# Performance work log

Measured on AMD Instinct MI355X. Metric: run time of the kernel, lower is better.

Reference implementation:

```python
import jax, jax.numpy as jnp
import numpy as np

DECAY = 0.99
EPS = 1e-05
TEMP = 1.0


def setup_inputs() -> dict:
    key = jax.random.key(0)
    k1, k2, k3 = jax.random.split(key, 3)
    B, T, D, C = 64, 512, 256, 1024
    x = jax.random.normal(k1, (B, T, D), dtype=jnp.float32)
    embed = jax.random.normal(k2, (1, C, D), dtype=jnp.float32)
    embed_avg = jax.random.normal(k3, (1, C, D), dtype=jnp.float32)
    cluster_size = jnp.ones((1, C), dtype=jnp.float32)
    return {"x": x, "embed": embed, "embed_avg": embed_avg, "cluster_size": cluster_size}


def reference(x, embed, embed_avg, cluster_size):
    B, T, D = x.shape
    H, C, _ = embed.shape  # H = num_codebooks = 1
    flatten = x.reshape(H, B * T, D)  # pack_one 'h * d'
    e = jax.lax.stop_gradient(embed)  # learnable_codebook = False

    dist = (2.0 * jnp.einsum('hnd,hcd->hnc', flatten, e)
            - jnp.sum(flatten * flatten, axis=-1, keepdims=True)
            - jnp.sum(e * e, axis=-1)[:, None, :])  # [h, N, C]

    # gumbel_sample: deterministic argmax + straight-through one-hot
    embed_ind = jnp.argmax(dist, axis=-1)  # [h, N]
    probs = jax.nn.softmax(dist / TEMP, axis=-1)
    hard = jax.nn.one_hot(embed_ind, C, dtype=dist.dtype)
    embed_onehot = probs + jax.lax.stop_gradient(hard - probs)  # [h, N, C]

    # quantize via onehot matmul (training path)
    quantize = jnp.einsum('hnc,hcd->hnd', embed_onehot, e).reshape(B, T, D)

    # EMA codebook update
    cs_new = DECAY * cluster_size + (1.0 - DECAY) * embed_onehot.sum(axis=1)  # [h, C]
    embed_sum = jnp.einsum('hnd,hnc->hcd', flatten, embed_onehot)  # [h, C, D]
    ea_new = DECAY * embed_avg + (1.0 - DECAY) * embed_sum
    n = jnp.sum(cs_new, axis=-1, keepdims=True)
    cs_smoothed = (cs_new + EPS) / (n + C * EPS) * n  # laplace smoothing * n
    embed_norm = ea_new / cs_smoothed[..., None]  # new codebook [h, C, D]

    return (quantize, embed_ind.reshape(B, T), embed_norm, cs_new)
```

## Files before the change

### kernel.cpp

```cpp
#include <hip/hip_runtime.h>
#include <cstdint>

#define DECAY 0.99f
#define OMD   0.01f
#define EPSV  1e-5f

constexpr int N_PTS   = 32768;
constexpr int D_DIM   = 256;
constexpr int C_CODES = 1024;
constexpr int NKT     = 12;
constexpr int AP      = 512;
constexpr int BP      = 512;

constexpr int PG = 8;
constexpr int PK = 8;
constexpr int LCAP = 4096;

typedef _Float16 half8  __attribute__((ext_vector_type(8)));
typedef _Float16 half4v __attribute__((ext_vector_type(4)));
typedef float    floatx4 __attribute__((ext_vector_type(4)));

constexpr size_t WS_ENORM = 0;
constexpr size_t WS_FCNT  = 1024;
constexpr size_t WS_XNORM = 2048;
constexpr size_t WS_PCNT  = 34816;
constexpr size_t WS_CAND4 = 43008;
constexpr size_t WS_FLAGR = WS_CAND4 + 1048576;
constexpr size_t WS_CAND2 = WS_FLAGR + 32768;
constexpr size_t WS_A16   = WS_CAND2 + 1048576;
constexpr size_t WS_B16   = WS_A16 + 8388608;
constexpr size_t WS_TOTAL_FLOATS = WS_B16 + 262144;

__device__ __forceinline__ void async_copy16(const void* g, void* s) {
    __builtin_amdgcn_global_load_lds(
        (const __attribute__((address_space(1))) unsigned int*)(uintptr_t)g,
        (__attribute__((address_space(3))) unsigned int*)(uintptr_t)s, 16, 0, 0);
}

__device__ __forceinline__ unsigned ord_u32(float v) {
    unsigned s = __float_as_uint(v);
    unsigned m = (unsigned)((int)s >> 31);
    return s ^ (m | 0x80000000u);
}
__device__ __forceinline__ float ord_dec(unsigned t) {
    unsigned s = (t & 0x80000000u) ? (t ^ 0x80000000u) : ~t;
    return __uint_as_float(s);
}

__global__ __launch_bounds__(256) void vq_prep(const float* __restrict__ X,
                                               const float* __restrict__ E,
                                               _Float16* __restrict__ A,
                                               _Float16* __restrict__ B,
                                               float* __restrict__ enorm,
                                               float* __restrict__ xnorm,
                                               int* __restrict__ fcnt) {
    if (blockIdx.x < 8192) {
        int i = blockIdx.x * 256 + threadIdx.x;
        int n = i >> 6, kq = (i & 63) * 4;
        float4 v = reinterpret_cast<const float4*>(X)[i];
        _Float16 h0 = (_Float16)v.x, h1 = (_Float16)v.y, h2 = (_Float16)v.z, h3 = (_Float16)v.w;
        _Float16 l0 = (_Float16)(v.x - (float)h0), l1 = (_Float16)(v.y - (float)h1);
        _Float16 l2 = (_Float16)(v.z - (float)h2), l3 = (_Float16)(v.w - (float)h3);
        half4v hi = {h0, h1, h2, h3};
        half4v lo = {l0, l1, l2, l3};
        _Float16* row = A + (size_t)n * AP;
        *reinterpret_cast<half4v*>(row + kq)       = hi;
        *reinterpret_cast<half4v*>(row + 256 + kq) = lo;
        float s = v.x * v.x + v.y * v.y + v.z * v.z + v.w * v.w;
        int lane = threadIdx.x & 63;
#pragma unroll
        for (int off = 32; off > 0; off >>= 1) s += __shfl_down(s, off, 64);
        if (lane == 0) xnorm[n] = s;
    } else {
        if (blockIdx.x == 8192 && threadIdx.x == 0) *fcnt = 0;
        int i = (blockIdx.x - 8192) * 256 + threadIdx.x;
        int c = i >> 6, kq = (i & 63) * 4;
        float4 v = reinterpret_cast<const float4*>(E)[i];
        _Float16 h0 = (_Float16)v.x, h1 = (_Float16)v.y, h2 = (_Float16)v.z, h3 = (_Float16)v.w;
        _Float16 l0 = (_Float16)(v.x - (float)h0), l1 = (_Float16)(v.y - (float)h1);
        _Float16 l2 = (_Float16)(v.z - (float)h2), l3 = (_Float16)(v.w - (float)h3);
        half4v hi = {h0, h1, h2, h3};
        half4v lo = {l0, l1, l2, l3};
        _Float16* row = B + (size_t)c * BP;
        *reinterpret_cast<half4v*>(row + kq)       = hi;
        *reinterpret_cast<half4v*>(row + 256 + kq) = lo;
        float s = v.x * v.x + v.y * v.y + v.z * v.z + v.w * v.w;
        int lane = threadIdx.x & 63;
#pragma unroll
        for (int off = 32; off > 0; off >>= 1) s += __shfl_down(s, off, 64);
        if (lane == 0) enorm[c] = s;
    }
}

__global__ __launch_bounds__(256) void vq_enorm(const float* __restrict__ E,
                                                float* __restrict__ enorm) {
    int c    = blockIdx.x * 4 + (threadIdx.x >> 6);
    int lane = threadIdx.x & 63;
    float4 v = reinterpret_cast<const float4*>(E)[c * 64 + lane];
    float s  = v.x * v.x + v.y * v.y + v.z * v.z + v.w * v.w;
#pragma unroll
    for (int off = 32; off > 0; off >>= 1) s += __shfl_down(s, off, 64);
    if (lane == 0) enorm[c] = s;
}

#define TOP2_DPP(CTRL)                                                          \
    {                                                                           \
        unsigned o1 = (unsigned)__builtin_amdgcn_update_dpp((int)k1, (int)k1,   \
                                                            CTRL, 0xF, 0xF, false); \
        unsigned o2 = (unsigned)__builtin_amdgcn_update_dpp((int)k2, (int)k2,   \
                                                            CTRL, 0xF, 0xF, false); \
        unsigned tmn = o1 < k1 ? o1 : k1;                                       \
        k1 = o1 > k1 ? o1 : k1;                                                 \
        k2 = o2 > k2 ? o2 : k2;                                                 \
        k2 = tmn > k2 ? tmn : k2;                                               \
    }

__global__ __launch_bounds__(256, 2) void vq_gemm1(
    const _Float16* __restrict__ A, const _Float16* __restrict__ B,
    const float* __restrict__ enorm, float4* __restrict__ cand4) {
    __shared__ _Float16 As[128 * 64];
    __shared__ _Float16 Bs[256 * 64];

    const int L  = blockIdx.x;
    const int ct = (L >> 3) & 3;
    const int rt = (L & 7) | ((L >> 5) << 3);
    const int n0  = rt * 128;
    const int cb0 = ct * 256;

    const int tid = threadIdx.x;
    const int w   = tid >> 6;
    const int l   = tid & 63;

    const int srow = l >> 3;
    const int sq   = (l & 7) ^ srow;

    floatx4 acc[4][8] = {};

    for (int kt = 0; kt < 4; ++kt) {
        const int k0 = kt * 64;
        __syncthreads();
#pragma unroll
        for (int t = 0; t < 4; ++t) {
            int rr = w * 32 + t * 8;
            const _Float16* ga = A + (size_t)(n0 + rr + srow) * AP + k0 + sq * 8;
            async_copy16(ga, &As[rr * 64]);
        }
#pragma unroll
        for (int t = 0; t < 8; ++t) {
            int rr = w * 64 + t * 8;
            const _Float16* gb = B + (size_t)(cb0 + rr + srow) * BP + k0 + sq * 8;
            async_copy16(gb, &Bs[rr * 64]);
        }
        __syncthreads();
#pragma unroll
        for (int kk = 0; kk < 2; ++kk) {
            half8 af[4], bf[8];
            int qa = kk * 4 + (l >> 4);
#pragma unroll
            for (int i = 0; i < 4; ++i) {
                int row = (w & 1) * 64 + 16 * i + (l & 15);
                af[i] = *reinterpret_cast<const half8*>(&As[row * 64 + (qa ^ (row & 7)) * 8]);
            }
#pragma unroll
            for (int j = 0; j < 8; ++j) {
                int crow = (w >> 1) * 128 + 16 * j + (l & 15);
                bf[j] = *reinterpret_cast<const half8*>(&Bs[crow * 64 + (qa ^ (crow & 7)) * 8]);
            }
#pragma unroll
            for (int i = 0; i < 4; ++i)
#pragma unroll
                for (int j = 0; j < 8; ++j)
                    acc[i][j] = __builtin_amdgcn_mfma_f32_16x16x32_f16(af[i], bf[j], acc[i][j], 0, 0, 0);
        }
    }

    const int colbase = cb0 + (w >> 1) * 128 + (l & 15);
    float    en[8];
    unsigned idxenc[8];
#pragma unroll
    for (int j = 0; j < 8; ++j) {
        en[j]     = enorm[colbase + 16 * j];
        idxenc[j] = 1023u - (unsigned)(colbase + 16 * j);
    }

#pragma unroll
    for (int i = 0; i < 4; ++i) {
#pragma unroll
        for (int reg = 0; reg < 4; ++reg) {
            unsigned k1 = 0u, k2 = 0u;
#pragma unroll
            for (int j = 0; j < 8; ++j) {
                float v = 2.0f * acc[i][j][reg] - en[j];
                unsigned key = (ord_u32(v) & 0xFFFFFC00u) | idxenc[j];
                unsigned tmn = key < k1 ? key : k1;
                k1 = key > k1 ? key : k1;
                k2 = tmn > k2 ? tmn : k2;
            }
            TOP2_DPP(0xB1)
            TOP2_DPP(0x4E)
            TOP2_DPP(0x141)
            TOP2_DPP(0x140)
            if ((l & 15) == 0) {
                unsigned c1 = 1023u - (k1 & 1023u);
                float v1 = ord_dec(k1 & 0xFFFFFC00u);
                float v2 = ord_dec(k2 & 0xFFFFFC00u);
                int row = n0 + (w & 1) * 64 + 16 * i + (l >> 4) * 4 + reg;
                cand4[(size_t)row * 8 + ct * 2 + (w >> 1)] =
                    make_float4(v1, (float)c1, v2, 0.0f);
            }
        }
    }
}

__global__ __launch_bounds__(256) void vq_merge3f(
    const float4* __restrict__ cand4, const float* __restrict__ E,
    const float* __restrict__ enorm, const float* __restrict__ xnorm,
    float* __restrict__ quant, float* __restrict__ indout,
    int* __restrict__ flagrows, int* __restrict__ fcnt) {
    __shared__ int   rowsel[64];
    __shared__ float emred[256];
    const int tid = threadIdx.x;
    const int n0  = blockIdx.x * 64;

    float em = fmaxf(fmaxf(enorm[tid], enorm[tid + 256]),
                     fmaxf(enorm[tid + 512], enorm[tid + 768]));
    emred[tid] = em;
    __syncthreads();
    for (int st = 128; st > 0; st >>= 1) {
        if (tid < st) emred[tid] = fmaxf(emred[tid], emred[tid + st]);
        __syncthreads();
    }
    const float emax = emred[0];

    if (tid < 64) {
        int r = n0 + tid;
        float b1 = -3.4e38f, b2 = -3.4e38f;
        int   i1 = 0x7fffffff;
#pragma unroll
        for (int t = 0; t < 8; ++t) {
            float4 cv = cand4[(size_t)r * 8 + t];
            int ci = (int)cv.y;
            if (cv.x > b1 || (cv.x == b1 && ci < i1)) { b2 = fmaxf(b1, cv.z); b1 = cv.x; i1 = ci; }
            else b2 = fmaxf(b2, cv.x);
        }
        i1 &= (C_CODES - 1);
        rowsel[tid] = i1;
        indout[r]   = (float)i1;
        float T = 0.004150390625f * sqrtf(xnorm[r] * emax)
                + 0.0001220703125f * emax + 0.5f;
        if (b1 - b2 <= T) { int p = atomicAdd(fcnt, 1); flagrows[p] = r; }
    }
    __syncthreads();

    const float4* E4 = reinterpret_cast<const float4*>(E);
    float4*       Q4 = reinterpret_cast<float4*>(quant);
    const int lane = tid & 63;
#pragma unroll
    for (int it = 0; it < 16; ++it) {
        int r   = (tid >> 6) + 4 * it;
        int idx = rowsel[r];
        Q4[(n0 + r) * 64 + lane] = E4[idx * 64 + lane];
    }
}

__global__ __launch_bounds__(256, 2) void vq_gemm2(
    const _Float16* __restrict__ A, const _Float16* __restrict__ B,
    const float* __restrict__ enorm, const int* __restrict__ flagrows,
    const int* __restrict__ fcnt, float2* __restrict__ cand2) {
    const int fc = *fcnt;

    const int L      = blockIdx.x;
    const int within = L >> 3;
    const int ct     = within & 7;
    const int rt     = (L & 7) | ((within >> 3) << 3);
    const int n0     = rt * 128;
    if (n0 >= fc) return;
    const int cb0    = ct * 128;

    __shared__ _Float16 As[128 * 64];
    __shared__ _Float16 Bs[128 * 64];

    const int tid = threadIdx.x;
    const int w   = tid >> 6;
    const int l   = tid & 63;
    const int srow = l >> 3;
    const int sq   = (l & 7) ^ srow;

    int grow[4];
#pragma unroll
    for (int t = 0; t < 4; ++t) {
        int slot = n0 + w * 32 + t * 8 + srow;
        int r    = (slot < fc) ? flagrows[slot] : 0;
        grow[t]  = r & (N_PTS - 1);
    }

    floatx4 acc[4][4] = {};

    for (int kt = 0; kt < NKT; ++kt) {
        const int ka = ((kt < 8) ? (kt & 3) : (kt - 4)) * 64;
        const int kb = (kt < 4) ? kt * 64 : (kt < 8 ? 256 + (kt - 4) * 64 : (kt - 8) * 64);
        __syncthreads();
#pragma unroll
        for (int t = 0; t < 4; ++t) {
            int rr = w * 32 + t * 8;
            const _Float16* ga = A + (size_t)grow[t] * AP + ka + sq * 8;
            async_copy16(ga, &As[rr * 64]);
            const _Float16* gb = B + (size_t)(cb0 + rr + srow) * BP + kb + sq * 8;
            async_copy16(gb, &Bs[rr * 64]);
        }
        __syncthreads();
#pragma unroll
        for (int kk = 0; kk < 2; ++kk) {
            half8 af[4], bf[4];
            int qa = kk * 4 + (l >> 4);
#pragma unroll
            for (int i = 0; i < 4; ++i) {
                int row  = (w & 1) * 64 + 16 * i + (l & 15);
                af[i] = *reinterpret_cast<const half8*>(&As[row * 64 + (qa ^ (row & 7)) * 8]);
                int crow = (w >> 1) * 64 + 16 * i + (l & 15);
                bf[i] = *reinterpret_cast<const half8*>(&Bs[crow * 64 + (qa ^ (crow & 7)) * 8]);
            }
#pragma unroll
            for (int i = 0; i < 4; ++i)
#pragma unroll
                for (int j = 0; j < 4; ++j)
                    acc[i][j] = __builtin_amdgcn_mfma_f32_16x16x32_f16(af[i], bf[j], acc[i][j], 0, 0, 0);
        }
    }

    const int colbase = cb0 + (w >> 1) * 64 + (l & 15);
    float en[4];
#pragma unroll
    for (int j = 0; j < 4; ++j) en[j] = enorm[colbase + 16 * j];

#pragma unroll
    for (int i = 0; i < 4; ++i) {
#pragma unroll
        for (int reg = 0; reg < 4; ++reg) {
            float bv = -3.4e38f;
            int   bi = 0x7fffffff;
#pragma unroll
            for (int j = 0; j < 4; ++j) {
                float v = 2.0f * acc[i][j][reg] - en[j];
                int   c = colbase + 16 * j;
                if (v > bv || (v == bv && c < bi)) { bv = v; bi = c; }
            }
#pragma unroll
            for (int s = 1; s < 16; s <<= 1) {
                float ov = __shfl_xor(bv, s, 64);
                int   oi = __shfl_xor(bi, s, 64);
                if (ov > bv || (ov == bv && oi < bi)) { bv = ov; bi = oi; }
            }
            if ((l & 15) == 0) {
                int slot = n0 + (w & 1) * 64 + 16 * i + (l >> 4) * 4 + reg;
                cand2[(size_t)slot * 16 + ct * 2 + (w >> 1)] = make_float2(bv, (float)bi);
            }
        }
    }
}

__global__ __launch_bounds__(256) void vq_patch(
    const float2* __restrict__ cand2, const int* __restrict__ flagrows,
    const int* __restrict__ fcnt, const float* __restrict__ E,
    float* __restrict__ quant, float* __restrict__ indout) {
    int fc = *fcnt;
    if (fc > N_PTS) fc = N_PTS;
    const int s0 = blockIdx.x * 64;
    if (s0 >= fc) return;

    __shared__ int rowsel[64];
    __shared__ int rowid[64];
    const int tid = threadIdx.x;
    if (tid < 64) {
        int s = s0 + tid;
        if (s < fc) {
            int r = flagrows[s] & (N_PTS - 1);
            float bv = -3.4e38f;
            int   bi = 0x7fffffff;
#pragma unroll
            for (int t = 0; t < 16; ++t) {
                float2 cv = cand2[(size_t)s * 16 + t];
                int ci = (int)cv.y;
                if (cv.x > bv || (cv.x == bv && ci < bi)) { bv = cv.x; bi = ci; }
            }
            bi &= (C_CODES - 1);
            rowsel[tid] = bi;
            rowid[tid]  = r;
            indout[r]   = (float)bi;
        } else {
            rowsel[tid] = -1;
            rowid[tid]  = 0;
        }
    }
    __syncthreads();

    const float4* E4 = reinterpret_cast<const float4*>(E);
    float4*       Q4 = reinterpret_cast<float4*>(quant);
    const int lane = tid & 63;
#pragma unroll
    for (int it = 0; it < 16; ++it) {
        int rs  = (tid >> 6) + 4 * it;
        int idx = rowsel[rs];
        if (idx >= 0) Q4[(size_t)rowid[rs] * 64 + lane] = E4[idx * 64 + lane];
    }
}

__global__ __launch_bounds__(256) void vq_part(
    const float* __restrict__ X, const float* __restrict__ indf,
    float* __restrict__ P, int* __restrict__ pcnt) {
    __shared__ int list[LCAP];
    __shared__ int cnt[PK];
    __shared__ int lcnt;
    const int cg = blockIdx.x;
    const int g  = blockIdx.y;
    const int t  = threadIdx.x;
    if (t == 0) lcnt = 0;
    if (t < PK) cnt[t] = 0;
    __syncthreads();

    const float4* I4 = reinterpret_cast<const float4*>(indf);
    float4 v[4];
#pragma unroll
    for (int j = 0; j < 4; ++j)
        v[j] = I4[g * 1024 + j * 256 + t];

#pragma unroll
    for (int j = 0; j < 4; ++j) {
        int base = (g * 1024 + j * 256 + t) * 4;
        int k0 = (int)v[j].x, k1 = (int)v[j].y, k2 = (int)v[j].z, k3 = (int)v[j].w;
        if ((k0 >> 3) == cg) { int p = atomicAdd(&lcnt, 1); atomicAdd(&cnt[k0 & 7], 1); if (p < LCAP) list[p] = ((base + 0) << 3) | (k0 & 7); }
        if ((k1 >> 3) == cg) { int p = atomicAdd(&lcnt, 1); atomicAdd(&cnt[k1 & 7], 1); if (p < LCAP) list[p] = ((base + 1) << 3) | (k1 & 7); }
        if ((k2 >> 3) == cg) { int p = atomicAdd(&lcnt, 1); atomicAdd(&cnt[k2 & 7], 1); if (p < LCAP) list[p] = ((base + 2) << 3) | (k2 & 7); }
        if ((k3 >> 3) == cg) { int p = atomicAdd(&lcnt, 1); atomicAdd(&cnt[k3 & 7], 1); if (p < LCAP) list[p] = ((base + 3) << 3) | (k3 & 7); }
    }
    __syncthreads();

    int m = lcnt; if (m > LCAP) m = LCAP;
    float acc[PK] = {0, 0, 0, 0, 0, 0, 0, 0};
    int r = 0;
    for (; r + 8 <= m; r += 8) {
        int e[8];
        float val[8];
#pragma unroll
        for (int q = 0; q < 8; ++q) e[q] = list[r + q];
#pragma unroll
        for (int q = 0; q < 8; ++q) val[q] = X[(size_t)(e[q] >> 3) * D_DIM + t];
#pragma unroll
        for (int q = 0; q < 8; ++q) {
            int k = e[q] & 7;
#pragma unroll
            for (int kk = 0; kk < PK; ++kk) acc[kk] += (k == kk) ? val[q] : 0.0f;
        }
    }
    for (; r < m; ++r) {
        int e = list[r];
        float val = X[(size_t)(e >> 3) * D_DIM + t];
        int k = e & 7;
#pragma unroll
        for (int kk = 0; kk < PK; ++kk) acc[kk] += (k == kk) ? val : 0.0f;
    }

#pragma unroll
    for (int kk = 0; kk < PK; ++kk)
        P[((size_t)g * C_CODES + cg * PK + kk) * D_DIM + t] = acc[kk];
    if (t < PK) pcnt[g * C_CODES + cg * PK + t] = cnt[t];
}

__global__ __launch_bounds__(256) void vq_comb(
    const float* __restrict__ P, const int* __restrict__ pcnt,
    const float* __restrict__ ea, const float* __restrict__ cs_in,
    float* __restrict__ emb_norm, float* __restrict__ cs_out) {
    __shared__ float red[256];
    const int c = blockIdx.x;
    const int t = threadIdx.x;
    red[t] = cs_in[t] + cs_in[t + 256] + cs_in[t + 512] + cs_in[t + 768];
    __syncthreads();
    for (int st = 128; st > 0; st >>= 1) {
        if (t < st) red[t] += red[t + st];
        __syncthreads();
    }
    const float cssum = red[0];

    float s = 0.0f;
#pragma unroll
    for (int g = 0; g < PG; ++g)
        s += P[((size_t)g * C_CODES + c) * D_DIM + t];
    int total = 0;
#pragma unroll
    for (int g = 0; g < PG; ++g) total += pcnt[g * C_CODES + c];
    float cs    = DECAY * cs_in[c] + OMD * (float)total;
    float ntot  = DECAY * cssum + OMD * (float)N_PTS;
    float denom = (cs + EPSV) / (ntot + (float)C_CODES * EPSV) * ntot;
    emb_norm[(size_t)c * D_DIM + t] =
        (DECAY * ea[(size_t)c * D_DIM + t] + OMD * s) / denom;
    if (t == 0) cs_out[c] = cs;
}

__global__ __launch_bounds__(256) void vq_main_fb(
    const float* __restrict__ X, const float* __restrict__ E,
    const float* __restrict__ enorm,
    float* __restrict__ quant, float* __restrict__ indout,
    float* __restrict__ counts, float* __restrict__ esum) {
    constexpr int BN = 64, BC = 64, BK = 32, PADR = 68;
    __shared__ float As[BK * PADR];
    __shared__ float Bs[BK * PADR];
    __shared__ float redv[BN * 16];
    __shared__ int   redi[BN * 16];
    __shared__ int   rowsel[BN];

    const int tid = threadIdx.x;
    const int n0  = blockIdx.x * BN;
    const int tr  = tid >> 4;
    const int tc  = tid & 15;
    const int sr  = tid >> 2;
    const int sk  = tid & 3;

    const float4* X4 = reinterpret_cast<const float4*>(X);
    const float4* E4 = reinterpret_cast<const float4*>(E);

    float best[4];
    int   bidx[4];
#pragma unroll
    for (int i = 0; i < 4; i++) { best[i] = -3.4e38f; bidx[i] = 0; }

    for (int c0 = 0; c0 < C_CODES; c0 += BC) {
        float acc[4][4] = {};
        for (int k0 = 0; k0 < D_DIM; k0 += BK) {
            __syncthreads();
#pragma unroll
            for (int it = 0; it < 2; ++it) {
                int   k4 = sk + 4 * it;
                float4 av = X4[(n0 + sr) * 64 + (k0 >> 2) + k4];
                float4 bv = E4[(c0 + sr) * 64 + (k0 >> 2) + k4];
                int kk = k4 * 4;
                As[(kk + 0) * PADR + sr] = av.x;
                As[(kk + 1) * PADR + sr] = av.y;
                As[(kk + 2) * PADR + sr] = av.z;
                As[(kk + 3) * PADR + sr] = av.w;
                Bs[(kk + 0) * PADR + sr] = bv.x;
                Bs[(kk + 1) * PADR + sr] = bv.y;
                Bs[(kk + 2) * PADR + sr] = bv.z;
                Bs[(kk + 3) * PADR + sr] = bv.w;
            }
            __syncthreads();
#pragma unroll
            for (int k = 0; k < BK; ++k) {
                float4 a = *reinterpret_cast<const float4*>(&As[k * PADR + 4 * tr]);
                float4 b = *reinterpret_cast<const float4*>(&Bs[k * PADR + 4 * tc]);
                acc[0][0] += a.x * b.x; acc[0][1] += a.x * b.y;
                acc[0][2] += a.x * b.z; acc[0][3] += a.x * b.w;
                acc[1][0] += a.y * b.x; acc[1][1] += a.y * b.y;
                acc[1][2] += a.y * b.z; acc[1][3] += a.y * b.w;
                acc[2][0] += a.z * b.x; acc[2][1] += a.z * b.y;
                acc[2][2] += a.z * b.z; acc[2][3] += a.z * b.w;
                acc[3][0] += a.w * b.x; acc[3][1] += a.w * b.y;
                acc[3][2] += a.w * b.z; acc[3][3] += a.w * b.w;
            }
        }
        float4 en = *reinterpret_cast<const float4*>(&enorm[c0 + 4 * tc]);
        float enj[4] = {en.x, en.y, en.z, en.w};
#pragma unroll
        for (int i = 0; i < 4; i++)
#pragma unroll
            for (int j = 0; j < 4; j++) {
                float v = 2.0f * acc[i][j] - enj[j];
                int   c = c0 + 4 * tc + j;
                if (v > best[i]) { best[i] = v; bidx[i] = c; }
            }
    }

    __syncthreads();
#pragma unroll
    for (int i = 0; i < 4; i++) {
        redv[(4 * tr + i) * 16 + tc] = best[i];
        redi[(4 * tr + i) * 16 + tc] = bidx[i];
    }
    __syncthreads();
    if (tid < BN) {
        float bv = redv[tid * 16];
        int   bi = redi[tid * 16];
        for (int t = 1; t < 16; t++) {
            float v  = redv[tid * 16 + t];
            int   id = redi[tid * 16 + t];
            if (v > bv || (v == bv && id < bi)) { bv = v; bi = id; }
        }
        rowsel[tid] = bi;
        indout[n0 + tid] = (float)bi;
        unsafeAtomicAdd(&counts[bi], 1.0f);
    }
    __syncthreads();

    float4*   Q4   = reinterpret_cast<float4*>(quant);
    const int lane = tid & 63;
#pragma unroll
    for (int it = 0; it < 16; ++it) {
        int r   = (tid >> 6) + 4 * it;
        int idx = rowsel[r];
        float4 ev = E4[idx * 64 + lane];
        Q4[(n0 + r) * 64 + lane] = ev;
        float4 xv = X4[(n0 + r) * 64 + lane];
        float* dst = &esum[idx * D_DIM + lane * 4];
        unsafeAtomicAdd(dst + 0, xv.x);
        unsafeAtomicAdd(dst + 1, xv.y);
        unsafeAtomicAdd(dst + 2, xv.z);
        unsafeAtomicAdd(dst + 3, xv.w);
    }
}

__global__ __launch_bounds__(1024) void vq_fin1(const float* __restrict__ cs_in,
                                                const float* __restrict__ counts,
                                                float* __restrict__ cs_out,
                                                float* __restrict__ denom) {
    __shared__ float red[1024];
    int   c  = threadIdx.x;
    float cs = DECAY * cs_in[c] + OMD * counts[c];
    cs_out[c] = cs;
    red[c]    = cs;
    __syncthreads();
    for (int s = 512; s > 0; s >>= 1) {
        if (c < s) red[c] += red[c + s];
        __syncthreads();
    }
    float ntot = red[0];
    denom[c] = (cs + EPSV) / (ntot + (float)C_CODES * EPSV) * ntot;
}

__global__ __launch_bounds__(256) void vq_fin2(const float* __restrict__ ea,
                                               const float* __restrict__ esum,
                                               const float* __restrict__ denom,
                                               float* __restrict__ out) {
    int i = blockIdx.x * 256 + threadIdx.x;
    int c = i >> 6;
    float4 a = reinterpret_cast<const float4*>(ea)[i];
    float4 s = reinterpret_cast<const float4*>(esum)[i];
    float  d = denom[c];
    float4 o;
    o.x = (DECAY * a.x + OMD * s.x) / d;
    o.y = (DECAY * a.y + OMD * s.y) / d;
    o.z = (DECAY * a.z + OMD * s.z) / d;
    o.w = (DECAY * a.w + OMD * s.w) / d;
    reinterpret_cast<float4*>(out)[i] = o;
}

extern "C" void kernel_launch(void* const* d_in, const int* in_sizes, int n_in,
                              void* d_out, int out_size, void* d_ws, size_t ws_size,
                              hipStream_t stream) {
    const float* x            = (const float*)d_in[0];
    const float* embed        = (const float*)d_in[1];
    const float* embed_avg    = (const float*)d_in[2];
    const float* cluster_size = (const float*)d_in[3];

    float* out      = (float*)d_out;
    float* quant    = out;
    float* ind      = out + (size_t)N_PTS * D_DIM;
    float* emb_norm = ind + N_PTS;
    float* cs_out   = emb_norm + (size_t)C_CODES * D_DIM;

    float* ws    = (float*)d_ws;
    float* enorm = ws + WS_ENORM;

    if (ws_size >= WS_TOTAL_FLOATS * sizeof(float)) {
        int*      fcnt  = (int*)(ws + WS_FCNT);
        int*      pcnt  = (int*)(ws + WS_PCNT);
        float*    xnorm = ws + WS_XNORM;
        float4*   cand4 = (float4*)(ws + WS_CAND4);
        float*    P     = ws + WS_CAND4;
        int*      flagr = (int*)(ws + WS_FLAGR);
        float2*   cand2 = (float2*)(ws + WS_CAND2);
        _Float16* A16   = (_Float16*)(ws + WS_A16);
        _Float16* B16   = (_Float16*)(ws + WS_B16);

        vq_prep<<<8448, 256, 0, stream>>>(x, embed, A16, B16, enorm, xnorm, fcnt);
        vq_gemm1<<<1024, 256, 0, stream>>>(A16, B16, enorm, cand4);
        vq_merge3f<<<N_PTS / 64, 256, 0, stream>>>(cand4, embed, enorm, xnorm,
                                                   quant, ind, flagr, fcnt);
        vq_gemm2<<<2048, 256, 0, stream>>>(A16, B16, enorm, flagr, fcnt, cand2);
        vq_patch<<<N_PTS / 64, 256, 0, stream>>>(cand2, flagr, fcnt, embed, quant, ind);
        vq_part<<<dim3(C_CODES / PK, PG), 256, 0, stream>>>(x, ind, P, pcnt);
        vq_comb<<<C_CODES, 256, 0, stream>>>(P, pcnt, embed_avg, cluster_size,
                                             emb_norm, cs_out);
    } else {
        vq_enorm<<<C_CODES / 4, 256, 0, stream>>>(embed, enorm);
        float* countsf = ws + WS_CAND4;
        float* esum    = ws + WS_CAND4 + 1024;
        float* denom   = ws + WS_A16;
        hipMemsetAsync(countsf, 0, (1024 + (size_t)C_CODES * D_DIM) * sizeof(float), stream);
        vq_main_fb<<<N_PTS / 64, 256, 0, stream>>>(x, embed, enorm, quant, ind, countsf, esum);
        vq_fin1<<<1, 1024, 0, stream>>>(cluster_size, countsf, cs_out, denom);
        vq_fin2<<<(C_CODES * D_DIM / 4) / 256, 256, 0, stream>>>(embed_avg, esum, denom, emb_norm);
    }
}
```

Before: 196.8 us.

## Fuse merge, patch and combine stages into GEMM/partial kernels via last-block counters

Each follow-up kernel (merge after gemm1, patch after gemm2, comb after part) is folded into the preceding kernel. The last block to finish a row tile or code group, detected through an atomic done-counter, performs the reduction. gemm2 now reduces candidates with 64-bit atomicMax keys instead of writing a candidate array for a separate patch pass. This removes three kernel launches and some intermediate traffic, at the cost of threadfences, atomics, and tail work serialized in a single block per tile.

```diff
diff --git a/kernel.cpp b/kernel.cpp
--- a/kernel.cpp
+++ b/kernel.cpp
@@ -22,12 +22,13 @@
 
 constexpr size_t WS_ENORM = 0;
 constexpr size_t WS_FCNT  = 1024;
+constexpr size_t WS_DCTL  = 1056;
 constexpr size_t WS_XNORM = 2048;
 constexpr size_t WS_PCNT  = 34816;
 constexpr size_t WS_CAND4 = 43008;
 constexpr size_t WS_FLAGR = WS_CAND4 + 1048576;
-constexpr size_t WS_CAND2 = WS_FLAGR + 32768;
-constexpr size_t WS_A16   = WS_CAND2 + 1048576;
+constexpr size_t WS_KEY64 = WS_FLAGR + 32768;
+constexpr size_t WS_A16   = WS_CAND4 + 2097152;
 constexpr size_t WS_B16   = WS_A16 + 8388608;
 constexpr size_t WS_TOTAL_FLOATS = WS_B16 + 262144;
 
@@ -53,7 +54,8 @@
                                                _Float16* __restrict__ B,
                                                float* __restrict__ enorm,
                                                float* __restrict__ xnorm,
-                                               int* __restrict__ fcnt) {
+                                               int* __restrict__ fcnt,
+                                               int* __restrict__ dctl) {
     if (blockIdx.x < 8192) {
         int i = blockIdx.x * 256 + threadIdx.x;
         int n = i >> 6, kq = (i & 63) * 4;
@@ -72,8 +74,11 @@
         for (int off = 32; off > 0; off >>= 1) s += __shfl_down(s, off, 64);
         if (lane == 0) xnorm[n] = s;
     } else {
-        if (blockIdx.x == 8192 && threadIdx.x == 0) *fcnt = 0;
-        int i = (blockIdx.x - 8192) * 256 + threadIdx.x;
+        int eb = blockIdx.x - 8192;
+        if (eb == 0) { if (threadIdx.x == 0) *fcnt = 0; dctl[threadIdx.x] = 0; }
+        else if (eb == 1) dctl[256 + threadIdx.x] = 0;
+        else if (eb == 2 && threadIdx.x < 128) dctl[512 + threadIdx.x] = 0;
+        int i = eb * 256 + threadIdx.x;
         int c = i >> 6, kq = (i & 63) * 4;
         float4 v = reinterpret_cast<const float4*>(E)[i];
         _Float16 h0 = (_Float16)v.x, h1 = (_Float16)v.y, h2 = (_Float16)v.z, h3 = (_Float16)v.w;
@@ -115,9 +120,13 @@
         k2 = tmn > k2 ? tmn : k2;                                               \
     }
 
-__global__ __launch_bounds__(256, 2) void vq_gemm1(
+__global__ __launch_bounds__(256, 2) void vq_gemm1m(
     const _Float16* __restrict__ A, const _Float16* __restrict__ B,
-    const float* __restrict__ enorm, float4* __restrict__ cand4) {
+    const float* __restrict__ enorm, float4* __restrict__ cand4,
+    const float* __restrict__ E, const float* __restrict__ xnorm,
+    float* __restrict__ quant, float* __restrict__ indout,
+    int* __restrict__ flagrows, int* __restrict__ fcnt,
+    unsigned long long* __restrict__ keyarr, int* __restrict__ done1) {
     __shared__ _Float16 As[128 * 64];
     __shared__ _Float16 Bs[256 * 64];
 
@@ -130,7 +139,6 @@
     const int tid = threadIdx.x;
     const int w   = tid >> 6;
     const int l   = tid & 63;
-
     const int srow = l >> 3;
     const int sq   = (l & 7) ^ srow;
 
@@ -210,18 +218,16 @@
             }
         }
     }
-}
-
-__global__ __launch_bounds__(256) void vq_merge3f(
-    const float4* __restrict__ cand4, const float* __restrict__ E,
-    const float* __restrict__ enorm, const float* __restrict__ xnorm,
-    float* __restrict__ quant, float* __restrict__ indout,
-    int* __restrict__ flagrows, int* __restrict__ fcnt) {
-    __shared__ int   rowsel[64];
+
+    __shared__ int amlast;
+    __threadfence();
+    if (tid == 0) amlast = (atomicAdd(&done1[rt], 1) == 3) ? 1 : 0;
+    __syncthreads();
+    if (!amlast) return;
+    __threadfence();
+
+    __shared__ int   rowsel[128];
     __shared__ float emred[256];
-    const int tid = threadIdx.x;
-    const int n0  = blockIdx.x * 64;
-
     float em = fmaxf(fmaxf(enorm[tid], enorm[tid + 256]),
                      fmaxf(enorm[tid + 512], enorm[tid + 768]));
     emred[tid] = em;
@@ -232,7 +238,7 @@
     }
     const float emax = emred[0];
 
-    if (tid < 64) {
+    if (tid < 128) {
         int r = n0 + tid;
         float b1 = -3.4e38f, b2 = -3.4e38f;
         int   i1 = 0x7fffffff;
@@ -248,7 +254,11 @@
         indout[r]   = (float)i1;
         float T = 0.004150390625f * sqrtf(xnorm[r] * emax)
                 + 0.0001220703125f * emax + 0.5f;
-        if (b1 - b2 <= T) { int p = atomicAdd(fcnt, 1); flagrows[p] = r; }
+        if (b1 - b2 <= T) {
+            int p = atomicAdd(fcnt, 1);
+            flagrows[p] = r;
+            keyarr[p]   = 0ull;
+        }
     }
     __syncthreads();
 
@@ -256,17 +266,19 @@
     float4*       Q4 = reinterpret_cast<float4*>(quant);
     const int lane = tid & 63;
 #pragma unroll
-    for (int it = 0; it < 16; ++it) {
+    for (int it = 0; it < 32; ++it) {
         int r   = (tid >> 6) + 4 * it;
         int idx = rowsel[r];
-        Q4[(n0 + r) * 64 + lane] = E4[idx * 64 + lane];
-    }
-}
-
-__global__ __launch_bounds__(256, 2) void vq_gemm2(
+        Q4[(size_t)(n0 + r) * 64 + lane] = E4[idx * 64 + lane];
+    }
+}
+
+__global__ __launch_bounds__(256, 2) void vq_gemm2p(
     const _Float16* __restrict__ A, const _Float16* __restrict__ B,
     const float* __restrict__ enorm, const int* __restrict__ flagrows,
-    const int* __restrict__ fcnt, float2* __restrict__ cand2) {
+    const int* __restrict__ fcnt, unsigned long long* __restrict__ keyarr,
+    const float* __restrict__ E, float* __restrict__ quant,
+    float* __restrict__ indout, int* __restrict__ done2) {
     const int fc = *fcnt;
 
     const int L      = blockIdx.x;
@@ -353,40 +365,31 @@
             }
             if ((l & 15) == 0) {
                 int slot = n0 + (w & 1) * 64 + 16 * i + (l >> 4) * 4 + reg;
-                cand2[(size_t)slot * 16 + ct * 2 + (w >> 1)] = make_float2(bv, (float)bi);
-            }
-        }
-    }
-}
-
-__global__ __launch_bounds__(256) void vq_patch(
-    const float2* __restrict__ cand2, const int* __restrict__ flagrows,
-    const int* __restrict__ fcnt, const float* __restrict__ E,
-    float* __restrict__ quant, float* __restrict__ indout) {
-    int fc = *fcnt;
-    if (fc > N_PTS) fc = N_PTS;
-    const int s0 = blockIdx.x * 64;
-    if (s0 >= fc) return;
-
-    __shared__ int rowsel[64];
-    __shared__ int rowid[64];
-    const int tid = threadIdx.x;
-    if (tid < 64) {
-        int s = s0 + tid;
-        if (s < fc) {
-            int r = flagrows[s] & (N_PTS - 1);
-            float bv = -3.4e38f;
-            int   bi = 0x7fffffff;
-#pragma unroll
-            for (int t = 0; t < 16; ++t) {
-                float2 cv = cand2[(size_t)s * 16 + t];
-                int ci = (int)cv.y;
-                if (cv.x > bv || (cv.x == bv && ci < bi)) { bv = cv.x; bi = ci; }
-            }
-            bi &= (C_CODES - 1);
-            rowsel[tid] = bi;
+                unsigned long long key =
+                    ((unsigned long long)ord_u32(bv) << 10) | (1023u - (unsigned)bi);
+                atomicMax(&keyarr[slot], key);
+            }
+        }
+    }
+
+    __shared__ int amlast;
+    __threadfence();
+    if (tid == 0) amlast = (atomicAdd(&done2[rt], 1) == 7) ? 1 : 0;
+    __syncthreads();
+    if (!amlast) return;
+    __threadfence();
+
+    __shared__ int rowsel[128];
+    __shared__ int rowid[128];
+    const int hi = (fc - n0 < 128) ? (fc - n0) : 128;
+    if (tid < 128) {
+        if (tid < hi) {
+            unsigned long long k = keyarr[n0 + tid];
+            int c = (int)(1023u - (unsigned)(k & 1023u)) & (C_CODES - 1);
+            int r = flagrows[n0 + tid] & (N_PTS - 1);
+            rowsel[tid] = c;
             rowid[tid]  = r;
-            indout[r]   = (float)bi;
+            indout[r]   = (float)c;
         } else {
             rowsel[tid] = -1;
             rowid[tid]  = 0;
@@ -398,16 +401,19 @@
     float4*       Q4 = reinterpret_cast<float4*>(quant);
     const int lane = tid & 63;
 #pragma unroll
-    for (int it = 0; it < 16; ++it) {
+    for (int it = 0; it < 32; ++it) {
         int rs  = (tid >> 6) + 4 * it;
         int idx = rowsel[rs];
         if (idx >= 0) Q4[(size_t)rowid[rs] * 64 + lane] = E4[idx * 64 + lane];
     }
 }
 
-__global__ __launch_bounds__(256) void vq_part(
+__global__ __launch_bounds__(256) void vq_partc(
     const float* __restrict__ X, const float* __restrict__ indf,
-    float* __restrict__ P, int* __restrict__ pcnt) {
+    float* __restrict__ P, int* __restrict__ pcnt,
+    const float* __restrict__ ea, const float* __restrict__ cs_in,
+    float* __restrict__ emb_norm, float* __restrict__ cs_out,
+    int* __restrict__ done3) {
     __shared__ int list[LCAP];
     __shared__ int cnt[PK];
     __shared__ int lcnt;
@@ -464,15 +470,15 @@
     for (int kk = 0; kk < PK; ++kk)
         P[((size_t)g * C_CODES + cg * PK + kk) * D_DIM + t] = acc[kk];
     if (t < PK) pcnt[g * C_CODES + cg * PK + t] = cnt[t];
-}
-
-__global__ __launch_bounds__(256) void vq_comb(
-    const float* __restrict__ P, const int* __restrict__ pcnt,
-    const float* __restrict__ ea, const float* __restrict__ cs_in,
-    float* __restrict__ emb_norm, float* __restrict__ cs_out) {
+
+    __shared__ int amlast;
+    __threadfence();
+    if (t == 0) amlast = (atomicAdd(&done3[cg], 1) == PG - 1) ? 1 : 0;
+    __syncthreads();
+    if (!amlast) return;
+    __threadfence();
+
     __shared__ float red[256];
-    const int c = blockIdx.x;
-    const int t = threadIdx.x;
     red[t] = cs_in[t] + cs_in[t + 256] + cs_in[t + 512] + cs_in[t + 768];
     __syncthreads();
     for (int st = 128; st > 0; st >>= 1) {
@@ -480,20 +486,24 @@
         __syncthreads();
     }
     const float cssum = red[0];
-
-    float s = 0.0f;
-#pragma unroll
-    for (int g = 0; g < PG; ++g)
-        s += P[((size_t)g * C_CODES + c) * D_DIM + t];
-    int total = 0;
-#pragma unroll
-    for (int g = 0; g < PG; ++g) total += pcnt[g * C_CODES + c];
-    float cs    = DECAY * cs_in[c] + OMD * (float)total;
-    float ntot  = DECAY * cssum + OMD * (float)N_PTS;
-    float denom = (cs + EPSV) / (ntot + (float)C_CODES * EPSV) * ntot;
-    emb_norm[(size_t)c * D_DIM + t] =
-        (DECAY * ea[(size_t)c * D_DIM + t] + OMD * s) / denom;
-    if (t == 0) cs_out[c] = cs;
+    const float ntot  = DECAY * cssum + OMD * (float)N_PTS;
+
+#pragma unroll
+    for (int kk = 0; kk < PK; ++kk) {
+        const int c = cg * PK + kk;
+        float s = 0.0f;
+        int total = 0;
+#pragma unroll
+        for (int gg = 0; gg < PG; ++gg) {
+            s     += P[((size_t)gg * C_CODES + c) * D_DIM + t];
+            total += pcnt[gg * C_CODES + c];
+        }
+        float cs    = DECAY * cs_in[c] + OMD * (float)total;
+        float denom = (cs + EPSV) / (ntot + (float)C_CODES * EPSV) * ntot;
+        emb_norm[(size_t)c * D_DIM + t] =
+            (DECAY * ea[(size_t)c * D_DIM + t] + OMD * s) / denom;
+        if (t == 0) cs_out[c] = cs;
+    }
 }
 
 __global__ __launch_bounds__(256) void vq_main_fb(
@@ -661,24 +671,23 @@
 
     if (ws_size >= WS_TOTAL_FLOATS * sizeof(float)) {
         int*      fcnt  = (int*)(ws + WS_FCNT);
+        int*      dctl  = (int*)(ws + WS_DCTL);
         int*      pcnt  = (int*)(ws + WS_PCNT);
         float*    xnorm = ws + WS_XNORM;
         float4*   cand4 = (float4*)(ws + WS_CAND4);
         float*    P     = ws + WS_CAND4;
         int*      flagr = (int*)(ws + WS_FLAGR);
-        float2*   cand2 = (float2*)(ws + WS_CAND2);
+        unsigned long long* key64 = (unsigned long long*)(ws + WS_KEY64);
         _Float16* A16   = (_Float16*)(ws + WS_A16);
         _Float16* B16   = (_Float16*)(ws + WS_B16);
 
-        vq_prep<<<8448, 256, 0, stream>>>(x, embed, A16, B16, enorm, xnorm, fcnt);
-        vq_gemm1<<<1024, 256, 0, stream>>>(A16, B16, enorm, cand4);
-        vq_merge3f<<<N_PTS / 64, 256, 0, stream>>>(cand4, embed, enorm, xnorm,
-                                                   quant, ind, flagr, fcnt);
-        vq_gemm2<<<2048, 256, 0, stream>>>(A16, B16, enorm, flagr, fcnt, cand2);
-        vq_patch<<<N_PTS / 64, 256, 0, stream>>>(cand2, flagr, fcnt, embed, quant, ind);
-        vq_part<<<dim3(C_CODES / PK, PG), 256, 0, stream>>>(x, ind, P, pcnt);
-        vq_comb<<<C_CODES, 256, 0, stream>>>(P, pcnt, embed_avg, cluster_size,
-                                             emb_norm, cs_out);
+        vq_prep<<<8448, 256, 0, stream>>>(x, embed, A16, B16, enorm, xnorm, fcnt, dctl);
+        vq_gemm1m<<<1024, 256, 0, stream>>>(A16, B16, enorm, cand4, embed, xnorm,
+                                            quant, ind, flagr, fcnt, key64, dctl);
+        vq_gemm2p<<<2048, 256, 0, stream>>>(A16, B16, enorm, flagr, fcnt, key64,
+                                            embed, quant, ind, dctl + 256);
+        vq_partc<<<dim3(C_CODES / PK, PG), 256, 0, stream>>>(
+            x, ind, P, pcnt, embed_avg, cluster_size, emb_norm, cs_out, dctl + 512);
     } else {
         vq_enorm<<<C_CODES / 4, 256, 0, stream>>>(embed, enorm);
         float* countsf = ws + WS_CAND4;
```

Result: slower. 448.5 us (+127.9%).

## Recompute x low-half in gemm2 and merge refinement candidates via 64-bit atomicMax

Applied to the files above, without the earlier changes.

The prep kernel now stores only the fp16 high part of x, halving the A workspace and its write traffic. The refinement GEMM rebuilds the low part on the fly from fp32 x for flagged rows. The per-tile candidate array and its 16-way merge loop are replaced by one packed 64-bit key per flagged row, updated with atomicMax, so the patch kernel reads a single value. This trades prep-time stores for extra conversion work and atomics in gemm2, and the partial-sum buffer is moved into the shrunken A region.

```diff
diff --git a/kernel.cpp b/kernel.cpp
--- a/kernel.cpp
+++ b/kernel.cpp
@@ -9,7 +9,7 @@
 constexpr int D_DIM   = 256;
 constexpr int C_CODES = 1024;
 constexpr int NKT     = 12;
-constexpr int AP      = 512;
+constexpr int AP      = 256;
 constexpr int BP      = 512;
 
 constexpr int PG = 8;
@@ -26,9 +26,9 @@
 constexpr size_t WS_PCNT  = 34816;
 constexpr size_t WS_CAND4 = 43008;
 constexpr size_t WS_FLAGR = WS_CAND4 + 1048576;
-constexpr size_t WS_CAND2 = WS_FLAGR + 32768;
-constexpr size_t WS_A16   = WS_CAND2 + 1048576;
-constexpr size_t WS_B16   = WS_A16 + 8388608;
+constexpr size_t WS_KEY64 = WS_FLAGR + 32768;
+constexpr size_t WS_A16   = WS_KEY64 + 65536;
+constexpr size_t WS_B16   = WS_A16 + 4194304;
 constexpr size_t WS_TOTAL_FLOATS = WS_B16 + 262144;
 
 __device__ __forceinline__ void async_copy16(const void* g, void* s) {
@@ -45,6 +45,11 @@
 __device__ __forceinline__ float ord_dec(unsigned t) {
     unsigned s = (t & 0x80000000u) ? (t ^ 0x80000000u) : ~t;
     return __uint_as_float(s);
+}
+
+__device__ __forceinline__ _Float16 lo_h(float f) {
+    _Float16 h = (_Float16)f;
+    return (_Float16)(f - (float)h);
 }
 
 __global__ __launch_bounds__(256) void vq_prep(const float* __restrict__ X,
@@ -59,13 +64,8 @@
         int n = i >> 6, kq = (i & 63) * 4;
         float4 v = reinterpret_cast<const float4*>(X)[i];
         _Float16 h0 = (_Float16)v.x, h1 = (_Float16)v.y, h2 = (_Float16)v.z, h3 = (_Float16)v.w;
-        _Float16 l0 = (_Float16)(v.x - (float)h0), l1 = (_Float16)(v.y - (float)h1);
-        _Float16 l2 = (_Float16)(v.z - (float)h2), l3 = (_Float16)(v.w - (float)h3);
         half4v hi = {h0, h1, h2, h3};
-        half4v lo = {l0, l1, l2, l3};
-        _Float16* row = A + (size_t)n * AP;
-        *reinterpret_cast<half4v*>(row + kq)       = hi;
-        *reinterpret_cast<half4v*>(row + 256 + kq) = lo;
+        *reinterpret_cast<half4v*>(A + (size_t)n * AP + kq) = hi;
         float s = v.x * v.x + v.y * v.y + v.z * v.z + v.w * v.w;
         int lane = threadIdx.x & 63;
 #pragma unroll
@@ -77,8 +77,7 @@
         int c = i >> 6, kq = (i & 63) * 4;
         float4 v = reinterpret_cast<const float4*>(E)[i];
         _Float16 h0 = (_Float16)v.x, h1 = (_Float16)v.y, h2 = (_Float16)v.z, h3 = (_Float16)v.w;
-        _Float16 l0 = (_Float16)(v.x - (float)h0), l1 = (_Float16)(v.y - (float)h1);
-        _Float16 l2 = (_Float16)(v.z - (float)h2), l3 = (_Float16)(v.w - (float)h3);
+        _Float16 l0 = lo_h(v.x), l1 = lo_h(v.y), l2 = lo_h(v.z), l3 = lo_h(v.w);
         half4v hi = {h0, h1, h2, h3};
         half4v lo = {l0, l1, l2, l3};
         _Float16* row = B + (size_t)c * BP;
@@ -216,7 +215,8 @@
     const float4* __restrict__ cand4, const float* __restrict__ E,
     const float* __restrict__ enorm, const float* __restrict__ xnorm,
     float* __restrict__ quant, float* __restrict__ indout,
-    int* __restrict__ flagrows, int* __restrict__ fcnt) {
+    int* __restrict__ flagrows, int* __restrict__ fcnt,
+    unsigned long long* __restrict__ keyarr) {
     __shared__ int   rowsel[64];
     __shared__ float emred[256];
     const int tid = threadIdx.x;
@@ -248,7 +248,11 @@
         indout[r]   = (float)i1;
         float T = 0.004150390625f * sqrtf(xnorm[r] * emax)
                 + 0.0001220703125f * emax + 0.5f;
-        if (b1 - b2 <= T) { int p = atomicAdd(fcnt, 1); flagrows[p] = r; }
+        if (b1 - b2 <= T) {
+            int p = atomicAdd(fcnt, 1);
+            flagrows[p] = r;
+            keyarr[p]   = 0ull;
+        }
     }
     __syncthreads();
 
@@ -265,8 +269,9 @@
 
 __global__ __launch_bounds__(256, 2) void vq_gemm2(
     const _Float16* __restrict__ A, const _Float16* __restrict__ B,
-    const float* __restrict__ enorm, const int* __restrict__ flagrows,
-    const int* __restrict__ fcnt, float2* __restrict__ cand2) {
+    const float* __restrict__ X, const float* __restrict__ enorm,
+    const int* __restrict__ flagrows, const int* __restrict__ fcnt,
+    unsigned long long* __restrict__ keyarr) {
     const int fc = *fcnt;
 
     const int L      = blockIdx.x;
@@ -300,13 +305,30 @@
         const int ka = ((kt < 8) ? (kt & 3) : (kt - 4)) * 64;
         const int kb = (kt < 4) ? kt * 64 : (kt < 8 ? 256 + (kt - 4) * 64 : (kt - 8) * 64);
         __syncthreads();
-#pragma unroll
-        for (int t = 0; t < 4; ++t) {
-            int rr = w * 32 + t * 8;
-            const _Float16* ga = A + (size_t)grow[t] * AP + ka + sq * 8;
-            async_copy16(ga, &As[rr * 64]);
-            const _Float16* gb = B + (size_t)(cb0 + rr + srow) * BP + kb + sq * 8;
-            async_copy16(gb, &Bs[rr * 64]);
+        if (kt < 8) {
+#pragma unroll
+            for (int t = 0; t < 4; ++t) {
+                int rr = w * 32 + t * 8;
+                const _Float16* ga = A + (size_t)grow[t] * AP + ka + sq * 8;
+                async_copy16(ga, &As[rr * 64]);
+                const _Float16* gb = B + (size_t)(cb0 + rr + srow) * BP + kb + sq * 8;
+                async_copy16(gb, &Bs[rr * 64]);
+            }
+        } else {
+            const int kx = ka - 256;
+#pragma unroll
+            for (int t = 0; t < 4; ++t) {
+                int rr = w * 32 + t * 8;
+                const float* xr = X + (size_t)grow[t] * D_DIM + kx + sq * 8;
+                float4 xa = *reinterpret_cast<const float4*>(xr);
+                float4 xb = *reinterpret_cast<const float4*>(xr + 4);
+                half8 hv;
+                hv[0] = lo_h(xa.x); hv[1] = lo_h(xa.y); hv[2] = lo_h(xa.z); hv[3] = lo_h(xa.w);
+                hv[4] = lo_h(xb.x); hv[5] = lo_h(xb.y); hv[6] = lo_h(xb.z); hv[7] = lo_h(xb.w);
+                *reinterpret_cast<half8*>(&As[rr * 64 + l * 8]) = hv;
+                const _Float16* gb = B + (size_t)(cb0 + rr + srow) * BP + kb + sq * 8;
+                async_copy16(gb, &Bs[rr * 64]);
+            }
         }
         __syncthreads();
 #pragma unroll
@@ -353,14 +375,16 @@
             }
             if ((l & 15) == 0) {
                 int slot = n0 + (w & 1) * 64 + 16 * i + (l >> 4) * 4 + reg;
-                cand2[(size_t)slot * 16 + ct * 2 + (w >> 1)] = make_float2(bv, (float)bi);
+                unsigned long long key =
+                    ((unsigned long long)ord_u32(bv) << 10) | (1023u - (unsigned)bi);
+                atomicMax(&keyarr[slot], key);
             }
         }
     }
 }
 
 __global__ __launch_bounds__(256) void vq_patch(
-    const float2* __restrict__ cand2, const int* __restrict__ flagrows,
+    const unsigned long long* __restrict__ keyarr, const int* __restrict__ flagrows,
     const int* __restrict__ fcnt, const float* __restrict__ E,
     float* __restrict__ quant, float* __restrict__ indout) {
     int fc = *fcnt;
@@ -374,19 +398,12 @@
     if (tid < 64) {
         int s = s0 + tid;
         if (s < fc) {
+            unsigned long long k = keyarr[s];
+            int c = (int)(1023u - (unsigned)(k & 1023u)) & (C_CODES - 1);
             int r = flagrows[s] & (N_PTS - 1);
-            float bv = -3.4e38f;
-            int   bi = 0x7fffffff;
-#pragma unroll
-            for (int t = 0; t < 16; ++t) {
-                float2 cv = cand2[(size_t)s * 16 + t];
-                int ci = (int)cv.y;
-                if (cv.x > bv || (cv.x == bv && ci < bi)) { bv = cv.x; bi = ci; }
-            }
-            bi &= (C_CODES - 1);
-            rowsel[tid] = bi;
+            rowsel[tid] = c;
             rowid[tid]  = r;
-            indout[r]   = (float)bi;
+            indout[r]   = (float)c;
         } else {
             rowsel[tid] = -1;
             rowid[tid]  = 0;
@@ -664,18 +681,18 @@
         int*      pcnt  = (int*)(ws + WS_PCNT);
         float*    xnorm = ws + WS_XNORM;
         float4*   cand4 = (float4*)(ws + WS_CAND4);
-        float*    P     = ws + WS_CAND4;
         int*      flagr = (int*)(ws + WS_FLAGR);
-        float2*   cand2 = (float2*)(ws + WS_CAND2);
+        unsigned long long* key64 = (unsigned long long*)(ws + WS_KEY64);
         _Float16* A16   = (_Float16*)(ws + WS_A16);
         _Float16* B16   = (_Float16*)(ws + WS_B16);
+        float*    P     = ws + WS_A16;
 
         vq_prep<<<8448, 256, 0, stream>>>(x, embed, A16, B16, enorm, xnorm, fcnt);
         vq_gemm1<<<1024, 256, 0, stream>>>(A16, B16, enorm, cand4);
         vq_merge3f<<<N_PTS / 64, 256, 0, stream>>>(cand4, embed, enorm, xnorm,
-                                                   quant, ind, flagr, fcnt);
-        vq_gemm2<<<2048, 256, 0, stream>>>(A16, B16, enorm, flagr, fcnt, cand2);
-        vq_patch<<<N_PTS / 64, 256, 0, stream>>>(cand2, flagr, fcnt, embed, quant, ind);
+                                                   quant, ind, flagr, fcnt, key64);
+        vq_gemm2<<<2048, 256, 0, stream>>>(A16, B16, x, enorm, flagr, fcnt, key64);
+        vq_patch<<<N_PTS / 64, 256, 0, stream>>>(key64, flagr, fcnt, embed, quant, ind);
         vq_part<<<dim3(C_CODES / PK, PG), 256, 0, stream>>>(x, ind, P, pcnt);
         vq_comb<<<C_CODES, 256, 0, stream>>>(P, pcnt, embed_avg, cluster_size,
                                              emb_norm, cs_out);
```

New measurement: 200.2 us. No clear change (+1.7%).
